# Performance work log

Hardware: AMD Instinct MI355X
Metric: run time of the kernel (lower is better)

Reference implementation:

```python
import jax, jax.numpy as jnp
import numpy as np

L, H, D, DH, FF, V, MAXPOS, SENSE, ATT = 12, 12, 768, 64, 3072, 30522, 512, 64, 64


def layer_norm(x, g, b, eps=1e-12):
    mu = jnp.mean(x, axis=-1, keepdims=True)
    var = jnp.mean((x - mu) ** 2, axis=-1, keepdims=True)
    return (x - mu) / jnp.sqrt(var + eps) * g + b


def setup_inputs() -> dict:
    key = jax.random.key(0)
    ks = jax.random.split(key, 24)
    B, S = 32, 256
    s = 0.02
    inp = {
        "input_ids": jax.random.randint(ks[0], (B, S), 0, V, dtype=jnp.int32),
        "token_type_ids": jnp.zeros((B, S), jnp.int32),
        "attention_mask": jnp.ones((B, S), jnp.int32),
        "location": jax.random.randint(ks[1], (B,), 1, S, dtype=jnp.int32),
        "sense_emb": jax.random.normal(ks[2], (SENSE, D), jnp.float32),
        # embedding tables
        "word_emb": s * jax.random.normal(ks[3], (V, D), jnp.float32),
        "pos_emb": s * jax.random.normal(ks[4], (MAXPOS, D), jnp.float32),
        "type_emb": s * jax.random.normal(ks[5], (2, D), jnp.float32),
        "emb_ln_g": jnp.ones((D,), jnp.float32),
        "emb_ln_b": jnp.zeros((D,), jnp.float32),
        # stacked per-layer transformer weights [L, ...]
        "Wq": s * jax.random.normal(ks[6], (L, D, D), jnp.float32),
        "bq": jnp.zeros((L, D), jnp.float32),
        "Wk": s * jax.random.normal(ks[7], (L, D, D), jnp.float32),
        "bk": jnp.zeros((L, D), jnp.float32),
        "Wv": s * jax.random.normal(ks[8], (L, D, D), jnp.float32),
        "bv": jnp.zeros((L, D), jnp.float32),
        "Wo": s * jax.random.normal(ks[9], (L, D, D), jnp.float32),
        "bo": jnp.zeros((L, D), jnp.float32),
        "ln1_g": jnp.ones((L, D), jnp.float32),
        "ln1_b": jnp.zeros((L, D), jnp.float32),
        "W1": s * jax.random.normal(ks[10], (L, D, FF), jnp.float32),
        "b1": jnp.zeros((L, FF), jnp.float32),
        "W2": s * jax.random.normal(ks[11], (L, FF, D), jnp.float32),
        "b2": jnp.zeros((L, D), jnp.float32),
        "ln2_g": jnp.ones((L, D), jnp.float32),
        "ln2_b": jnp.zeros((L, D), jnp.float32),
        # SelfAttention(sense_num) projections, scale dim = 64
        "att_Wq": s * jax.random.normal(ks[12], (D, ATT), jnp.float32),
        "att_Wk": s * jax.random.normal(ks[13], (D, ATT), jnp.float32),
    }
    return inp


def bert_encode(input_ids, token_type_ids, attention_mask, word_emb, pos_emb,
                type_emb, emb_ln_g, emb_ln_b, Wq, bq, Wk, bk, Wv, bv, Wo, bo,
                ln1_g, ln1_b, W1, b1, W2, b2, ln2_g, ln2_b):
    B, S = input_ids.shape
    x = word_emb[input_ids] + pos_emb[:S][None, :, :] + type_emb[token_type_ids]
    x = layer_norm(x, emb_ln_g, emb_ln_b)
    # additive mask bias: [B,1,1,S]
    bias = (1.0 - attention_mask.astype(x.dtype))[:, None, None, :] * -10000.0
    scale = 1.0 / jnp.sqrt(jnp.asarray(DH, x.dtype))
    for l in range(L):
        q = (x @ Wq[l] + bq[l]).reshape(B, S, H, DH).transpose(0, 2, 1, 3)
        k = (x @ Wk[l] + bk[l]).reshape(B, S, H, DH).transpose(0, 2, 1, 3)
        v = (x @ Wv[l] + bv[l]).reshape(B, S, H, DH).transpose(0, 2, 1, 3)
        scores = jnp.einsum("bhqd,bhkd->bhqk", q, k) * scale + bias
        attn = jax.nn.softmax(scores, axis=-1)
        o = jnp.einsum("bhqk,bhkd->bhqd", attn, v)
        o = o.transpose(0, 2, 1, 3).reshape(B, S, D)
        x = layer_norm(x + o @ Wo[l] + bo[l], ln1_g[l], ln1_b[l])
        h = jax.nn.gelu(x @ W1[l] + b1[l], approximate=False)
        x = layer_norm(x + h @ W2[l] + b2[l], ln2_g[l], ln2_b[l])
    return x


def reference(input_ids, token_type_ids, attention_mask, location, sense_emb,
              word_emb, pos_emb, type_emb, emb_ln_g, emb_ln_b, Wq, bq, Wk, bk,
              Wv, bv, Wo, bo, ln1_g, ln1_b, W1, b1, W2, b2, ln2_g, ln2_b,
              att_Wq, att_Wk):
    last_layer = bert_encode(input_ids, token_type_ids, attention_mask,
                             word_emb, pos_emb, type_emb, emb_ln_g, emb_ln_b,
                             Wq, bq, Wk, bk, Wv, bv, Wo, bo, ln1_g, ln1_b,
                             W1, b1, W2, b2, ln2_g, ln2_b)
    B = last_layer.shape[0]
    # gather the pun-word embedding at `location[i]` per row  -> [B, D]
    pun = last_layer[jnp.arange(B), location]
    # SelfAttention(sense_num) with scale 64: scaled dot-product scores [B, SENSE]
    scores = (pun @ att_Wq) @ (sense_emb @ att_Wk).T / jnp.sqrt(jnp.asarray(ATT, pun.dtype))
    res = jax.nn.softmax(scores, axis=1)
    # fused top-2 (replaces the original per-scalar Python loop)
    _, idx = jax.lax.top_k(res, 2)
    return idx.astype(jnp.float32)
```

## Files before the change

kernel.cpp:

```cpp
#include <hip/hip_runtime.h>
#include <math.h>

typedef __attribute__((ext_vector_type(8))) short short8;
typedef __attribute__((ext_vector_type(8))) _Float16 half8;
typedef __attribute__((ext_vector_type(4))) float f32x4;

static constexpr int Lc = 12;
static constexpr int Hc = 12;
static constexpr int Dc = 768;
static constexpr int DHc = 64;
static constexpr int FFc = 3072;
static constexpr int SENSEc = 64;
static constexpr int ATTc = 64;
static constexpr int QS = 3 * Dc;
static constexpr int KPAD = 72;

__device__ __forceinline__ unsigned short f2h(float f) {
    _Float16 h = (_Float16)f;
    union { _Float16 h; unsigned short u; } c;
    c.h = h;
    return c.u;
}

__device__ __forceinline__ void load_lds16(const void* g, void* l) {
    __builtin_amdgcn_global_load_lds(
        (const __attribute__((address_space(1))) unsigned int*)g,
        (__attribute__((address_space(3))) unsigned int*)l, 16, 0, 0);
}

__device__ __forceinline__ float blockReduceSum256(float v, float* sred) {
#pragma unroll
    for (int off = 32; off > 0; off >>= 1) v += __shfl_down(v, off, 64);
    int lane = threadIdx.x & 63, wid = threadIdx.x >> 6;
    if (lane == 0) sred[wid] = v;
    __syncthreads();
    float total = sred[0] + sred[1] + sred[2] + sred[3];
    __syncthreads();
    return total;
}

__global__ __launch_bounds__(256) void embed_kernel(
    const int* __restrict__ ids, const int* __restrict__ tts,
    const float* __restrict__ we, const float* __restrict__ pe,
    const float* __restrict__ te, const float* __restrict__ g,
    const float* __restrict__ b, float* __restrict__ x,
    unsigned short* __restrict__ xh, int S)
{
    int tok = blockIdx.x, t = threadIdx.x;
    int ss = tok % S;
    int id = ids[tok], tt = tts[tok];
    __shared__ float sred[4];
    float v[3];
    float s = 0.f;
#pragma unroll
    for (int i = 0; i < 3; ++i) {
        int d = t + i * 256;
        v[i] = we[(size_t)id * Dc + d] + pe[(size_t)ss * Dc + d] + te[(size_t)tt * Dc + d];
        s += v[i];
    }
    float mu = blockReduceSum256(s, sred) * (1.f / Dc);
    float s2 = 0.f;
#pragma unroll
    for (int i = 0; i < 3; ++i) { v[i] -= mu; s2 += v[i] * v[i]; }
    float rstd = rsqrtf(blockReduceSum256(s2, sred) * (1.f / Dc) + 1e-12f);
    size_t ro = (size_t)tok * Dc;
#pragma unroll
    for (int i = 0; i < 3; ++i) {
        int d = t + i * 256;
        float val = v[i] * rstd * g[d] + b[d];
        x[ro + d] = val;
        xh[ro + d] = f2h(val);
    }
}

__global__ __launch_bounds__(256) void resln_kernel(
    float* __restrict__ x, const float* __restrict__ y,
    const float* __restrict__ g, const float* __restrict__ b,
    unsigned short* __restrict__ xh)
{
    int tok = blockIdx.x, t = threadIdx.x;
    __shared__ float sred[4];
    size_t ro = (size_t)tok * Dc;
    float v[3];
    float s = 0.f;
#pragma unroll
    for (int i = 0; i < 3; ++i) {
        int d = t + i * 256;
        v[i] = x[ro + d] + y[ro + d];
        s += v[i];
    }
    float mu = blockReduceSum256(s, sred) * (1.f / Dc);
    float s2 = 0.f;
#pragma unroll
    for (int i = 0; i < 3; ++i) { v[i] -= mu; s2 += v[i] * v[i]; }
    float rstd = rsqrtf(blockReduceSum256(s2, sred) * (1.f / Dc) + 1e-12f);
#pragma unroll
    for (int i = 0; i < 3; ++i) {
        int d = t + i * 256;
        float val = v[i] * rstd * g[d] + b[d];
        x[ro + d] = val;
        xh[ro + d] = f2h(val);
    }
}

__global__ __launch_bounds__(256) void convert_weights(
    const float* __restrict__ Wq, const float* __restrict__ Wk,
    const float* __restrict__ Wv, const float* __restrict__ Wo,
    const float* __restrict__ W1, const float* __restrict__ W2,
    unsigned short* __restrict__ qh, unsigned short* __restrict__ oh,
    unsigned short* __restrict__ h1, unsigned short* __restrict__ h2)
{
    int id = blockIdx.x;
    const float* src; unsigned short *dh; int Kd, Nd, tx, ty;
    if (id < 576) {
        int m = id / 144, tile = id % 144;
        src = (m == 0) ? Wq : (m == 1) ? Wk : (m == 2) ? Wv : Wo;
        if (m < 3) { dh = qh + (size_t)m * Dc * Dc; }
        else       { dh = oh; }
        Kd = Dc; Nd = Dc; tx = tile % 12; ty = tile / 12;
    } else if (id < 1152) {
        int tile = id - 576;
        src = W1; dh = h1; Kd = Dc; Nd = FFc; tx = tile % 48; ty = tile / 48;
    } else {
        int tile = id - 1152;
        src = W2; dh = h2; Kd = FFc; Nd = Dc; tx = tile % 12; ty = tile / 12;
    }
    int k0 = ty * 64, n0 = tx * 64;
    __shared__ float tileS[64][65];
    int t = threadIdx.x, c = t & 63, r0 = t >> 6;
#pragma unroll
    for (int i = 0; i < 16; ++i) {
        int kr = r0 + i * 4;
        tileS[kr][c] = src[(size_t)(k0 + kr) * Nd + n0 + c];
    }
    __syncthreads();
#pragma unroll
    for (int i = 0; i < 16; ++i) {
        int nr = r0 + i * 4;
        float v = tileS[c][nr];
        size_t idx = (size_t)(n0 + nr) * Kd + k0 + c;
        dh[idx] = f2h(v);
    }
}

__global__ __launch_bounds__(256) void biascat_kernel(
    const float* __restrict__ bq, const float* __restrict__ bk,
    const float* __restrict__ bv, float* __restrict__ out)
{
    int lyr = blockIdx.x, t = threadIdx.x;
    for (int j = t; j < QS; j += 256) {
        float v = (j < Dc) ? bq[lyr * Dc + j]
                : (j < 2 * Dc) ? bk[lyr * Dc + j - Dc]
                : bv[lyr * Dc + j - 2 * Dc];
        out[lyr * QS + j] = v;
    }
}

template <int MODE>
__global__ __launch_bounds__(256, 2) void mfma_gemm_f16(
    const unsigned short* __restrict__ Ah, const unsigned short* __restrict__ Bh,
    const float* __restrict__ bias, float* __restrict__ Cf,
    unsigned short* __restrict__ Ch, int M, int N, int K)
{
    __shared__ alignas(16) unsigned short Ash[2][128 * 64];
    __shared__ alignas(16) unsigned short Bsh[2][128 * 64];
    int t = threadIdx.x, w = t >> 6, l = t & 63;
    int m0 = blockIdx.y * 128, n0 = blockIdx.x * 128;
    int wm = (w >> 1) * 64, wn = (w & 1) * 64;
    int sw = (((l & 7) ^ (l >> 3)) << 3);
    size_t go = (size_t)(w * 8 + (l >> 3)) * K + sw;
    const unsigned short* gah = Ah + (size_t)m0 * K + go;
    const unsigned short* gbh = Bh + (size_t)n0 * K + go;
    int lo = w * 512 + l * 8;
    f32x4 acc[4][4];
#pragma unroll
    for (int i = 0; i < 4; ++i)
#pragma unroll
        for (int j = 0; j < 4; ++j) acc[i][j] = (f32x4)0.f;
    int fm = l & 15, grp = l >> 4;
    int axor = fm & 7;
    int nk = K >> 6;

#define STAGE_TILE(buf, k0)                                          \
    {                                                                \
        _Pragma("unroll")                                            \
        for (int i = 0; i < 4; ++i) {                                \
            size_t g = (size_t)(i * 32) * K + (k0);                  \
            int d = lo + i * 2048;                                   \
            load_lds16(gah + g, &Ash[buf][0] + d);                   \
            load_lds16(gbh + g, &Bsh[buf][0] + d);                   \
        }                                                            \
    }

    STAGE_TILE(0, 0);
    int cur = 0;
    for (int tk = 0; tk < nk; ++tk) {
        __builtin_amdgcn_s_barrier();
        __builtin_amdgcn_sched_barrier(0);
        if (tk + 1 < nk) {
            STAGE_TILE(cur ^ 1, (tk + 1) << 6);
            asm volatile("s_waitcnt vmcnt(8)" ::: "memory");
        } else {
            asm volatile("s_waitcnt vmcnt(0)" ::: "memory");
        }
        __builtin_amdgcn_s_barrier();
        __builtin_amdgcn_sched_barrier(0);
        const unsigned short* As = &Ash[cur][0];
        const unsigned short* Bs = &Bsh[cur][0];
#pragma unroll
        for (int h = 0; h < 2; ++h) {
            int koff = (((h * 4 + grp) ^ axor) << 3);
            half8 fa[4], fb[4];
#pragma unroll
            for (int i = 0; i < 4; ++i) {
                int ra = (wm + i * 16 + fm) * 64 + koff;
                int rb = (wn + i * 16 + fm) * 64 + koff;
                fa[i] = *(const half8*)(As + ra);
                fb[i] = *(const half8*)(Bs + rb);
            }
#pragma unroll
            for (int i = 0; i < 4; ++i)
#pragma unroll
                for (int j = 0; j < 4; ++j)
                    acc[i][j] = __builtin_amdgcn_mfma_f32_16x16x32_f16(
                        fa[i], fb[j], acc[i][j], 0, 0, 0);
        }
        cur ^= 1;
    }
#undef STAGE_TILE
    int col_l = l & 15, row_l = (l >> 4) * 4;
#pragma unroll
    for (int j = 0; j < 4; ++j) {
        int col = n0 + wn + j * 16 + col_l;
        float bcv = bias[col];
#pragma unroll
        for (int i = 0; i < 4; ++i) {
            int row = m0 + wm + i * 16 + row_l;
#pragma unroll
            for (int r = 0; r < 4; ++r) {
                float v = acc[i][j][r] + bcv;
                size_t idx = (size_t)(row + r) * N + col;
                if (MODE == 1) {
                    v = 0.5f * v * (1.f + erff(v * 0.70710678118654752f));
                    Ch[idx] = f2h(v);
                } else if (MODE == 2) {
                    Ch[idx] = f2h(v);
                } else {
                    Cf[idx] = v;
                }
            }
        }
    }
}

__global__ __launch_bounds__(256, 1) void attn_mfma(
    const unsigned short* __restrict__ qkv, const int* __restrict__ mask,
    unsigned short* __restrict__ aoh, int B, int S)
{
    int bh = blockIdx.x, b = bh / Hc, hd = bh % Hc;
    int t = threadIdx.x, w = t >> 6, l = t & 63;
    int grp = l >> 4, lc = l & 15;
    __shared__ alignas(16) unsigned short Ks[256 * 64];
    __shared__ alignas(16) unsigned short Vts[4][64 * KPAD];
    __shared__ alignas(16) unsigned short Pw[4][64 * KPAD];
    __shared__ float mb[256];
    size_t rowbase = (size_t)(b * S) * QS;

    mb[t] = (1.f - (float)mask[b * S + t]) * -10000.0f;

    for (int p = 0; p < 4; ++p) {
        int key = p * 64 + (t >> 2);
        int d0 = (t & 3) * 16;
        const unsigned short* ksrc = qkv + rowbase + (size_t)key * QS + Dc + hd * DHc + d0;
        short8 s0 = *(const short8*)ksrc;
        short8 s1 = *(const short8*)(ksrc + 8);
        int c0 = d0 >> 3;
        *(short8*)(Ks + key * 64 + (((c0 + 0) ^ (key & 7)) << 3)) = s0;
        *(short8*)(Ks + key * 64 + (((c0 + 1) ^ (key & 7)) << 3)) = s1;
        const unsigned short* vsrc = qkv + rowbase + (size_t)key * QS + 2 * Dc + hd * DHc + d0;
        short8 v0 = *(const short8*)vsrc;
        short8 v1 = *(const short8*)(vsrc + 8);
        int kk = t >> 2;
#pragma unroll
        for (int u = 0; u < 8; ++u) {
            Vts[p][(d0 + u) * KPAD + kk]     = (unsigned short)v0[u];
            Vts[p][(d0 + 8 + u) * KPAD + kk] = (unsigned short)v1[u];
        }
    }

    int q0 = w * 64;
    half8 qf[4][2];
#pragma unroll
    for (int i = 0; i < 4; ++i)
#pragma unroll
        for (int kc = 0; kc < 2; ++kc)
            qf[i][kc] = *(const half8*)(qkv + rowbase
                        + (size_t)(q0 + 16 * i + lc) * QS + hd * DHc + kc * 32 + grp * 8);
    __syncthreads();

    f32x4 oacc[4][4];
#pragma unroll
    for (int i = 0; i < 4; ++i)
#pragma unroll
        for (int j = 0; j < 4; ++j) oacc[i][j] = (f32x4)0.f;
    float mstate[4][4], lstate[4][4];
#pragma unroll
    for (int i = 0; i < 4; ++i)
#pragma unroll
        for (int r = 0; r < 4; ++r) { mstate[i][r] = -3.0e38f; lstate[i][r] = 0.f; }

    for (int c = 0; c < 4; ++c) {
        f32x4 sacc[4][4];
#pragma unroll
        for (int i = 0; i < 4; ++i)
#pragma unroll
            for (int j = 0; j < 4; ++j) sacc[i][j] = (f32x4)0.f;
#pragma unroll
        for (int kc = 0; kc < 2; ++kc) {
            half8 kf[4];
#pragma unroll
            for (int j = 0; j < 4; ++j) {
                int krow = c * 64 + 16 * j + lc;
                kf[j] = *(const half8*)(Ks + krow * 64 + (((kc * 4 + grp) ^ (lc & 7)) << 3));
            }
#pragma unroll
            for (int i = 0; i < 4; ++i)
#pragma unroll
                for (int j = 0; j < 4; ++j)
                    sacc[i][j] = __builtin_amdgcn_mfma_f32_16x16x32_f16(
                        qf[i][kc], kf[j], sacc[i][j], 0, 0, 0);
        }
#pragma unroll
        for (int j = 0; j < 4; ++j) {
            float mbv = mb[c * 64 + 16 * j + lc];
#pragma unroll
            for (int i = 0; i < 4; ++i)
#pragma unroll
                for (int r = 0; r < 4; ++r)
                    sacc[i][j][r] = sacc[i][j][r] * 0.125f + mbv;
        }
#pragma unroll
        for (int i = 0; i < 4; ++i)
#pragma unroll
            for (int r = 0; r < 4; ++r) {
                float cm = fmaxf(fmaxf(sacc[i][0][r], sacc[i][1][r]),
                                 fmaxf(sacc[i][2][r], sacc[i][3][r]));
#pragma unroll
                for (int mw = 1; mw < 16; mw <<= 1)
                    cm = fmaxf(cm, __shfl_xor(cm, mw, 16));
                float nm = fmaxf(mstate[i][r], cm);
                float alpha = expf(mstate[i][r] - nm);
                mstate[i][r] = nm;
                float rs = 0.f;
#pragma unroll
                for (int j = 0; j < 4; ++j) {
                    float p = expf(sacc[i][j][r] - nm);
                    sacc[i][j][r] = p;
                    rs += p;
                }
#pragma unroll
                for (int mw = 1; mw < 16; mw <<= 1)
                    rs += __shfl_xor(rs, mw, 16);
                lstate[i][r] = lstate[i][r] * alpha + rs;
#pragma unroll
                for (int j = 0; j < 4; ++j) oacc[i][j][r] *= alpha;
            }
#pragma unroll
        for (int i = 0; i < 4; ++i)
#pragma unroll
            for (int j = 0; j < 4; ++j)
#pragma unroll
                for (int r = 0; r < 4; ++r)
                    Pw[w][(16 * i + 4 * grp + r) * KPAD + 16 * j + lc] =
                        f2h(sacc[i][j][r]);
        __syncthreads();
#pragma unroll
        for (int kc = 0; kc < 2; ++kc) {
            half8 pf[4], vf[4];
#pragma unroll
            for (int i = 0; i < 4; ++i)
                pf[i] = *(const half8*)(&Pw[w][(16 * i + lc) * KPAD + kc * 32 + grp * 8]);
#pragma unroll
            for (int j = 0; j < 4; ++j)
                vf[j] = *(const half8*)(&Vts[c][(16 * j + lc) * KPAD + kc * 32 + grp * 8]);
#pragma unroll
            for (int i = 0; i < 4; ++i)
#pragma unroll
                for (int j = 0; j < 4; ++j)
                    oacc[i][j] = __builtin_amdgcn_mfma_f32_16x16x32_f16(
                        pf[i], vf[j], oacc[i][j], 0, 0, 0);
        }
        __syncthreads();
    }
#pragma unroll
    for (int i = 0; i < 4; ++i)
#pragma unroll
        for (int r = 0; r < 4; ++r) {
            float inv = 1.f / lstate[i][r];
            size_t tok = (size_t)(b * S + q0 + 16 * i + 4 * grp + r);
#pragma unroll
            for (int j = 0; j < 4; ++j) {
                float v = oacc[i][j][r] * inv;
                size_t idx = tok * Dc + hd * DHc + 16 * j + lc;
                aoh[idx] = f2h(v);
            }
        }
}

__global__ __launch_bounds__(64) void pun_proj_kernel(
    const float* __restrict__ x, const int* __restrict__ loc,
    const float* __restrict__ Wq, float* __restrict__ pq, int S)
{
    __shared__ float pun[Dc];
    int b = blockIdx.x, t = threadIdx.x;
    const float* row = x + ((size_t)b * S + loc[b]) * Dc;
    for (int i = t; i < Dc; i += 64) pun[i] = row[i];
    __syncthreads();
    float acc = 0.f;
    for (int d = 0; d < Dc; ++d) acc += pun[d] * Wq[(size_t)d * ATTc + t];
    pq[b * ATTc + t] = acc;
}

__global__ __launch_bounds__(64) void sense_proj_kernel(
    const float* __restrict__ se, const float* __restrict__ Wk,
    float* __restrict__ sk)
{
    __shared__ float srow[Dc];
    int i = blockIdx.x, t = threadIdx.x;
    const float* row = se + (size_t)i * Dc;
    for (int j = t; j < Dc; j += 64) srow[j] = row[j];
    __syncthreads();
    float acc = 0.f;
    for (int d = 0; d < Dc; ++d) acc += srow[d] * Wk[(size_t)d * ATTc + t];
    sk[i * ATTc + t] = acc;
}

__global__ __launch_bounds__(64) void top2_kernel(
    const float* __restrict__ pq, const float* __restrict__ sk,
    float* __restrict__ out)
{
    __shared__ float pqs[ATTc];
    __shared__ float scs[SENSEc];
    int b = blockIdx.x, t = threadIdx.x;
    pqs[t] = pq[b * ATTc + t];
    __syncthreads();
    float acc = 0.f;
#pragma unroll
    for (int d = 0; d < ATTc; ++d) acc += pqs[d] * sk[t * ATTc + d];
    scs[t] = acc;
    __syncthreads();
    if (t == 0) {
        float v1 = -INFINITY, v2 = -INFINITY;
        int i1 = 0, i2 = 0;
        for (int i = 0; i < SENSEc; ++i) {
            float s = scs[i];
            if (s > v1) { v2 = v1; i2 = i1; v1 = s; i1 = i; }
            else if (s > v2) { v2 = s; i2 = i; }
        }
        out[b * 2 + 0] = (float)i1;
        out[b * 2 + 1] = (float)i2;
    }
}

extern "C" void kernel_launch(void* const* d_in, const int* in_sizes, int n_in,
                              void* d_out, int out_size, void* d_ws, size_t ws_size,
                              hipStream_t stream)
{
    (void)n_in; (void)out_size; (void)ws_size;
    const int*   input_ids  = (const int*)d_in[0];
    const int*   token_type = (const int*)d_in[1];
    const int*   attn_mask  = (const int*)d_in[2];
    const int*   location   = (const int*)d_in[3];
    const float* sense_emb  = (const float*)d_in[4];
    const float* word_emb   = (const float*)d_in[5];
    const float* pos_emb    = (const float*)d_in[6];
    const float* type_emb   = (const float*)d_in[7];
    const float* eg         = (const float*)d_in[8];
    const float* eb         = (const float*)d_in[9];
    const float* Wq         = (const float*)d_in[10];
    const float* bq         = (const float*)d_in[11];
    const float* Wk         = (const float*)d_in[12];
    const float* bk         = (const float*)d_in[13];
    const float* Wv         = (const float*)d_in[14];
    const float* bv         = (const float*)d_in[15];
    const float* Wo         = (const float*)d_in[16];
    const float* bo         = (const float*)d_in[17];
    const float* ln1g       = (const float*)d_in[18];
    const float* ln1b       = (const float*)d_in[19];
    const float* W1         = (const float*)d_in[20];
    const float* b1         = (const float*)d_in[21];
    const float* W2         = (const float*)d_in[22];
    const float* b2         = (const float*)d_in[23];
    const float* ln2g       = (const float*)d_in[24];
    const float* ln2b       = (const float*)d_in[25];
    const float* attWq      = (const float*)d_in[26];
    const float* attWk      = (const float*)d_in[27];
    float* out = (float*)d_out;

    int B = in_sizes[3];
    int S = in_sizes[0] / B;
    int NT = B * S;
    size_t NTD = (size_t)NT * Dc;

    float*          x   = (float*)d_ws;
    unsigned short* xh  = (unsigned short*)(x + NTD);
    float*          y   = (float*)(xh + NTD);
    unsigned short* hh  = (unsigned short*)(y + NTD);
    unsigned short* qkv = hh;
    unsigned short* aoh = qkv + (size_t)NT * QS;
    float*          bc  = (float*)(hh + (size_t)NT * FFc);
    unsigned short* wqh = (unsigned short*)(bc + (size_t)Lc * QS);
    unsigned short* woh = wqh + (size_t)QS * Dc;
    unsigned short* w1h = woh + (size_t)Dc * Dc;
    unsigned short* w2h = w1h + (size_t)FFc * Dc;
    float*          pq  = (float*)(w2h + (size_t)Dc * FFc);
    float*          sk  = pq + (size_t)B * ATTc;

    embed_kernel<<<NT, 256, 0, stream>>>(input_ids, token_type, word_emb,
                                         pos_emb, type_emb, eg, eb, x, xh, S);
    biascat_kernel<<<Lc, 256, 0, stream>>>(bq, bk, bv, bc);

    dim3 gQKV(QS / 128, NT / 128);
    dim3 gD(Dc / 128, NT / 128);
    dim3 gF(FFc / 128, NT / 128);
    for (int l = 0; l < Lc; ++l) {
        convert_weights<<<1728, 256, 0, stream>>>(
            Wq + (size_t)l * Dc * Dc, Wk + (size_t)l * Dc * Dc,
            Wv + (size_t)l * Dc * Dc, Wo + (size_t)l * Dc * Dc,
            W1 + (size_t)l * Dc * FFc, W2 + (size_t)l * FFc * Dc,
            wqh, woh, w1h, w2h);
        mfma_gemm_f16<2><<<gQKV, 256, 0, stream>>>(
            xh, wqh, bc + (size_t)l * QS, nullptr, qkv, NT, QS, Dc);
        attn_mfma<<<B * Hc, 256, 0, stream>>>(qkv, attn_mask, aoh, B, S);
        mfma_gemm_f16<0><<<gD, 256, 0, stream>>>(
            aoh, woh, bo + (size_t)l * Dc, y, nullptr, NT, Dc, Dc);
        resln_kernel<<<NT, 256, 0, stream>>>(x, y, ln1g + (size_t)l * Dc,
                                             ln1b + (size_t)l * Dc, xh);
        mfma_gemm_f16<1><<<gF, 256, 0, stream>>>(
            xh, w1h, b1 + (size_t)l * FFc, nullptr, hh, NT, FFc, Dc);
        mfma_gemm_f16<0><<<gD, 256, 0, stream>>>(
            hh, w2h, b2 + (size_t)l * Dc, y, nullptr, NT, Dc, FFc);
        resln_kernel<<<NT, 256, 0, stream>>>(x, y, ln2g + (size_t)l * Dc,
                                             ln2b + (size_t)l * Dc, xh);
    }

    pun_proj_kernel<<<B, 64, 0, stream>>>(x, location, attWq, pq, S);
    sense_proj_kernel<<<SENSEc, 64, 0, stream>>>(sense_emb, attWk, sk);
    top2_kernel<<<B, 64, 0, stream>>>(pq, sk, out);
}
```

Before: 4.031 ms.

## Switch GEMM to triple-buffered BK=32 LDS pipeline with one barrier per step

```diff
diff --git a/kernel.cpp b/kernel.cpp
--- a/kernel.cpp
+++ b/kernel.cpp
@@ -157,18 +157,18 @@
 }
 
 template <int MODE>
-__global__ __launch_bounds__(256, 2) void mfma_gemm_f16(
+__global__ __launch_bounds__(256, 3) void mfma_gemm_f16(
     const unsigned short* __restrict__ Ah, const unsigned short* __restrict__ Bh,
     const float* __restrict__ bias, float* __restrict__ Cf,
     unsigned short* __restrict__ Ch, int M, int N, int K)
 {
-    __shared__ alignas(16) unsigned short Ash[2][128 * 64];
-    __shared__ alignas(16) unsigned short Bsh[2][128 * 64];
+    __shared__ alignas(16) unsigned short Ash[3][128 * 32];
+    __shared__ alignas(16) unsigned short Bsh[3][128 * 32];
     int t = threadIdx.x, w = t >> 6, l = t & 63;
     int m0 = blockIdx.y * 128, n0 = blockIdx.x * 128;
     int wm = (w >> 1) * 64, wn = (w & 1) * 64;
-    int sw = (((l & 7) ^ (l >> 3)) << 3);
-    size_t go = (size_t)(w * 8 + (l >> 3)) * K + sw;
+    int swc = (((l & 3) ^ ((l >> 3) & 3)) << 3);
+    size_t go = (size_t)(w * 16 + (l >> 2)) * K + swc;
     const unsigned short* gah = Ah + (size_t)m0 * K + go;
     const unsigned short* gbh = Bh + (size_t)n0 * K + go;
     int lo = w * 512 + l * 8;
@@ -178,56 +178,52 @@
 #pragma unroll
         for (int j = 0; j < 4; ++j) acc[i][j] = (f32x4)0.f;
     int fm = l & 15, grp = l >> 4;
-    int axor = fm & 7;
-    int nk = K >> 6;
-
-#define STAGE_TILE(buf, k0)                                          \
+    int koff = ((grp ^ ((fm >> 1) & 3)) << 3);
+    int nk = K >> 5;
+
+#define STAGE32(buf, tk)                                             \
     {                                                                \
         _Pragma("unroll")                                            \
-        for (int i = 0; i < 4; ++i) {                                \
-            size_t g = (size_t)(i * 32) * K + (k0);                  \
+        for (int i = 0; i < 2; ++i) {                                \
+            size_t g = (size_t)(i * 64) * K + (size_t)(tk) * 32;     \
             int d = lo + i * 2048;                                   \
             load_lds16(gah + g, &Ash[buf][0] + d);                   \
             load_lds16(gbh + g, &Bsh[buf][0] + d);                   \
         }                                                            \
     }
 
-    STAGE_TILE(0, 0);
+    STAGE32(0, 0);
+    STAGE32(1, 1);
     int cur = 0;
     for (int tk = 0; tk < nk; ++tk) {
+        if (tk < nk - 1) {
+            asm volatile("s_waitcnt vmcnt(4)" ::: "memory");
+        } else {
+            asm volatile("s_waitcnt vmcnt(0)" ::: "memory");
+        }
         __builtin_amdgcn_s_barrier();
         __builtin_amdgcn_sched_barrier(0);
-        if (tk + 1 < nk) {
-            STAGE_TILE(cur ^ 1, (tk + 1) << 6);
-            asm volatile("s_waitcnt vmcnt(8)" ::: "memory");
-        } else {
-            asm volatile("s_waitcnt vmcnt(0)" ::: "memory");
-        }
-        __builtin_amdgcn_s_barrier();
-        __builtin_amdgcn_sched_barrier(0);
+        if (tk + 2 < nk) {
+            int stg = cur - 1; if (stg < 0) stg += 3;
+            STAGE32(stg, tk + 2);
+        }
         const unsigned short* As = &Ash[cur][0];
         const unsigned short* Bs = &Bsh[cur][0];
-#pragma unroll
-        for (int h = 0; h < 2; ++h) {
-            int koff = (((h * 4 + grp) ^ axor) << 3);
-            half8 fa[4], fb[4];
-#pragma unroll
-            for (int i = 0; i < 4; ++i) {
-                int ra = (wm + i * 16 + fm) * 64 + koff;
-                int rb = (wn + i * 16 + fm) * 64 + koff;
-                fa[i] = *(const half8*)(As + ra);
-                fb[i] = *(const half8*)(Bs + rb);
-            }
-#pragma unroll
-            for (int i = 0; i < 4; ++i)
-#pragma unroll
-                for (int j = 0; j < 4; ++j)
-                    acc[i][j] = __builtin_amdgcn_mfma_f32_16x16x32_f16(
-                        fa[i], fb[j], acc[i][j], 0, 0, 0);
-        }
-        cur ^= 1;
-    }
-#undef STAGE_TILE
+        half8 fa[4], fb[4];
+#pragma unroll
+        for (int i = 0; i < 4; ++i) {
+            fa[i] = *(const half8*)(As + (wm + i * 16 + fm) * 32 + koff);
+            fb[i] = *(const half8*)(Bs + (wn + i * 16 + fm) * 32 + koff);
+        }
+#pragma unroll
+        for (int i = 0; i < 4; ++i)
+#pragma unroll
+            for (int j = 0; j < 4; ++j)
+                acc[i][j] = __builtin_amdgcn_mfma_f32_16x16x32_f16(
+                    fa[i], fb[j], acc[i][j], 0, 0, 0);
+        cur = (cur == 2) ? 0 : cur + 1;
+    }
+#undef STAGE32
     int col_l = l & 15, row_l = (l >> 4) * 4;
 #pragma unroll
     for (int j = 0; j < 4; ++j) {
```

New measurement: 4.220 ms. +4.7%, slower.
